# Optimization experiments

Hardware: AMD Instinct MI355X
Metric: run time of the kernel (lower is better)

The kernel has to match this reference:

```python
import jax, jax.numpy as jnp
import numpy as np

HEADS = 16

def setup_inputs() -> dict:
    key = jax.random.key(0)
    ks = jax.random.split(key, 5)
    B, T, D = 2, 2048, 2048
    s = 0.02
    return {
        "x": jax.random.normal(ks[0], (B, T, D), dtype=jnp.float32),
        "Wq": jax.random.normal(ks[1], (D, D), dtype=jnp.float32) * s,
        "Wk": jax.random.normal(ks[2], (D, D), dtype=jnp.float32) * s,
        "Wv": jax.random.normal(ks[3], (D, D), dtype=jnp.float32) * s,
        "Wo": jax.random.normal(ks[4], (D, D), dtype=jnp.float32) * s,
    }

def reference(x, Wq, Wk, Wv, Wo):
    B, T, _ = x.shape
    H = HEADS
    Dh = Wq.shape[1] // H
    # projections: [B,T,H,Dh]
    q = (x @ Wq).reshape(B, T, H, Dh)
    k = (x @ Wk).reshape(B, T, H, Dh)
    v = (x @ Wv).reshape(B, T, H, Dh)
    # raw scores [B,H,T,T]
    scores = jnp.einsum("bthd,bshd->bhts", q, k)
    # NOTE (faithful to source): mask is multiplicative 0/1 tril (the
    # masked_fill(-inf) in the torch code is not in-place and has no effect),
    # and the scale is sqrt(token_len), not sqrt(head_dim).
    mask = jnp.tril(jnp.ones((T, T), dtype=scores.dtype))
    scores = scores * mask
    attn = jax.nn.softmax(scores / (T ** 0.5), axis=-1)
    out = jnp.einsum("bhts,bshd->bthd", attn, v).reshape(B, T, H * Dh)
    return out @ Wo
```

## Files before the change

kernel.cpp:

```cpp
#include <hip/hip_runtime.h>


typedef __attribute__((ext_vector_type(4))) float  f32x4;
typedef __attribute__((ext_vector_type(8))) short  bf16x8;
typedef __attribute__((ext_vector_type(4))) unsigned short u16x4;

#define AS1 __attribute__((address_space(1)))
#define AS3 __attribute__((address_space(3)))

__device__ __forceinline__ void llds16(const void* g, void* l) {
  __builtin_amdgcn_global_load_lds((const AS1 void*)g, (AS3 void*)l, 16, 0, 0);
}

__device__ __forceinline__ unsigned short f2bf(float f) {
  unsigned int u = __builtin_bit_cast(unsigned int, f);
  u += 0x7fffu + ((u >> 16) & 1u);
  return (unsigned short)(u >> 16);
}

__device__ __forceinline__ unsigned short f2bfru(float f) {
  return (unsigned short)((__builtin_bit_cast(unsigned int, f) + 0x8000u) >> 16);
}

__device__ __forceinline__ float bf2f(unsigned short u) {
  return __builtin_bit_cast(float, (unsigned int)u << 16);
}

__global__ __launch_bounds__(256) void cast_x_kernel(const float* __restrict__ in,
                                                     unsigned short* __restrict__ out) {
  int i = blockIdx.x * 256 + threadIdx.x;
  f32x4 v = ((const f32x4*)in)[i];
  u16x4 o;
  o[0] = f2bf(v[0]); o[1] = f2bf(v[1]); o[2] = f2bf(v[2]); o[3] = f2bf(v[3]);
  ((u16x4*)out)[i] = o;
}

__global__ __launch_bounds__(256) void transpose_w4_kernel(
    const float* __restrict__ W0, const float* __restrict__ W1,
    const float* __restrict__ W2, const float* __restrict__ W3,
    unsigned short* __restrict__ T0, unsigned short* __restrict__ T1,
    unsigned short* __restrict__ T2, unsigned short* __restrict__ T3) {
  __shared__ float tile[32][33];
  const int z = blockIdx.z;
  const float* W = (z == 0) ? W0 : (z == 1) ? W1 : (z == 2) ? W2 : W3;
  unsigned short* Wt = (z == 0) ? T0 : (z == 1) ? T1 : (z == 2) ? T2 : T3;
  const int bx = blockIdx.x << 5;
  const int by = blockIdx.y << 5;
  const int tx = threadIdx.x;
  const int ty = threadIdx.y;
#pragma unroll
  for (int r = ty; r < 32; r += 8)
    tile[r][tx] = W[(size_t)(bx + r) * 2048 + by + tx];
  __syncthreads();
#pragma unroll
  for (int r = ty; r < 32; r += 8)
    Wt[(size_t)(by + r) * 2048 + bx + tx] = f2bf(tile[tx][r]);
}

__global__ __launch_bounds__(512, 2) void gemm_qkv8(const unsigned short* __restrict__ A,
                                                    const unsigned short* __restrict__ Bt,
                                                    unsigned short* __restrict__ Qb,
                                                    unsigned short* __restrict__ Kb,
                                                    unsigned short* __restrict__ Vt) {
  __shared__ __align__(16) char smem[131072];
  const int tid  = threadIdx.x;
  const int lane = tid & 63;
  const int w    = tid >> 6;
  const int wr   = w >> 2;
  const int wc   = w & 3;
  const int q16  = lane >> 4;
  const int l15  = lane & 15;
  const int f    = blockIdx.x;
  const int bn   = ((f & 7) << 1) + ((f >> 3) & 1);
  const int bm   = f >> 4;

  const int srow = tid >> 3;
  const int scl  = (tid & 7) ^ (srow & 7);
  const unsigned short* aS = A  + (size_t)((bm << 7) + srow) * 2048 + (scl << 3);
  const unsigned short* bS = Bt + (size_t)(bn * 384 + srow) * 2048 + (scl << 3);
  const int sdst = tid << 4;

  const int swzb = (q16 ^ (l15 & 7)) << 4;
  const int aRd  = ((wr << 6) + l15) << 7;
  const int bRd  = 16384 + ((wc * 96 + l15) << 7);

  f32x4 acc[4][6];
#pragma unroll
  for (int i = 0; i < 4; ++i)
#pragma unroll
    for (int j = 0; j < 6; ++j) acc[i][j] = (f32x4){0.f, 0.f, 0.f, 0.f};

  bf16x8 af[4], bf[3];

  auto TILE = [&](int kt, int cb, int ob, bool st) {
    const int kn = (kt + 1) << 6;
#pragma unroll
    for (int mi = 0; mi < 4; ++mi)
      af[mi] = *(const bf16x8*)(smem + cb + aRd + (mi << 11) + swzb);
#pragma unroll
    for (int r = 0; r < 3; ++r)
      bf[r] = *(const bf16x8*)(smem + cb + bRd + (r << 11) + swzb);
    if (st) {
      llds16(aS + kn,              smem + ob + sdst);
      llds16(aS + (1 << 17) + kn,  smem + ob + 8192 + sdst);
      llds16(bS + kn,              smem + ob + 16384 + sdst);
    }
    asm volatile("s_barrier" ::: "memory");
    __builtin_amdgcn_s_setprio(1);
#pragma unroll
    for (int mi = 0; mi < 4; ++mi)
#pragma unroll
      for (int r = 0; r < 3; ++r)
        acc[mi][r] = __builtin_amdgcn_mfma_f32_16x16x32_bf16(af[mi], bf[r], acc[mi][r], 0, 0, 0);
    __builtin_amdgcn_s_setprio(0);
    asm volatile("s_barrier" ::: "memory");
#pragma unroll
    for (int r = 0; r < 3; ++r)
      bf[r] = *(const bf16x8*)(smem + cb + bRd + ((3 + r) << 11) + swzb);
    if (st) {
      llds16(bS + (1 << 17) + kn,  smem + ob + 16384 + 8192 + sdst);
      llds16(bS + (2 << 17) + kn,  smem + ob + 16384 + 16384 + sdst);
      llds16(bS + (3 << 17) + kn,  smem + ob + 16384 + 24576 + sdst);
    }
    asm volatile("s_barrier" ::: "memory");
    __builtin_amdgcn_s_setprio(1);
#pragma unroll
    for (int mi = 0; mi < 4; ++mi)
#pragma unroll
      for (int r = 0; r < 3; ++r)
        acc[mi][3 + r] = __builtin_amdgcn_mfma_f32_16x16x32_bf16(af[mi], bf[r], acc[mi][3 + r], 0, 0, 0);
    __builtin_amdgcn_s_setprio(0);
    asm volatile("s_barrier" ::: "memory");
#pragma unroll
    for (int mi = 0; mi < 4; ++mi)
      af[mi] = *(const bf16x8*)(smem + cb + aRd + (mi << 11) + (swzb ^ 64));
#pragma unroll
    for (int r = 0; r < 3; ++r)
      bf[r] = *(const bf16x8*)(smem + cb + bRd + (r << 11) + (swzb ^ 64));
    if (st) {
      llds16(bS + (4 << 17) + kn,  smem + ob + 16384 + 32768 + sdst);
      llds16(bS + (5 << 17) + kn,  smem + ob + 16384 + 40960 + sdst);
    }
    asm volatile("s_barrier" ::: "memory");
    __builtin_amdgcn_s_setprio(1);
#pragma unroll
    for (int mi = 0; mi < 4; ++mi)
#pragma unroll
      for (int r = 0; r < 3; ++r)
        acc[mi][r] = __builtin_amdgcn_mfma_f32_16x16x32_bf16(af[mi], bf[r], acc[mi][r], 0, 0, 0);
    __builtin_amdgcn_s_setprio(0);
    asm volatile("s_barrier" ::: "memory");
#pragma unroll
    for (int r = 0; r < 3; ++r)
      bf[r] = *(const bf16x8*)(smem + cb + bRd + ((3 + r) << 11) + (swzb ^ 64));
    asm volatile("s_barrier" ::: "memory");
    __builtin_amdgcn_s_setprio(1);
#pragma unroll
    for (int mi = 0; mi < 4; ++mi)
#pragma unroll
      for (int r = 0; r < 3; ++r)
        acc[mi][3 + r] = __builtin_amdgcn_mfma_f32_16x16x32_bf16(af[mi], bf[r], acc[mi][3 + r], 0, 0, 0);
    __builtin_amdgcn_s_setprio(0);
    asm volatile("s_barrier" ::: "memory");
    asm volatile("s_waitcnt vmcnt(0)" ::: "memory");
    asm volatile("s_barrier" ::: "memory");
  };

  llds16(aS, smem + sdst);
  llds16(aS + (1 << 17), smem + 8192 + sdst);
#pragma unroll
  for (int li = 0; li < 6; ++li)
    llds16(bS + li * (1 << 17), smem + 16384 + li * 8192 + sdst);
  asm volatile("s_waitcnt vmcnt(0)" ::: "memory");
  asm volatile("s_barrier" ::: "memory");

#pragma unroll 1
  for (int kt = 0; kt < 30; kt += 2) {
    TILE(kt,     0,     65536, true);
    TILE(kt + 1, 65536, 0,     true);
  }
  TILE(30, 0,     65536, true);
  TILE(31, 65536, 0,     false);

  const float qscale = 0.02209708691207961f;
  const int rb = q16 << 2;
#pragma unroll
  for (int mi = 0; mi < 4; ++mi) {
    int m0 = (bm << 7) + (wr << 6) + (mi << 4) + rb;
#pragma unroll
    for (int ni = 0; ni < 6; ++ni) {
      int gn = bn * 384 + wc * 96 + (ni << 4) + l15;
      int region = gn >> 11;
      int nloc = gn & 2047;
      if (region == 0) {
#pragma unroll
        for (int j = 0; j < 4; ++j)
          Qb[(size_t)(m0 + j) * 2048 + nloc] = f2bf(acc[mi][ni][j] * qscale);
      } else if (region == 1) {
#pragma unroll
        for (int j = 0; j < 4; ++j)
          Kb[(size_t)(m0 + j) * 2048 + nloc] = f2bf(acc[mi][ni][j]);
      } else {
        u16x4 pk;
#pragma unroll
        for (int j = 0; j < 4; ++j) pk[j] = f2bf(acc[mi][ni][j]);
        int b = m0 >> 11, t = m0 & 2047;
        *(u16x4*)(Vt + ((size_t)((b << 4) + (nloc >> 7)) * 128 + (nloc & 127)) * 2048 + t) = pk;
      }
    }
  }
}

__global__ __launch_bounds__(256, 2) void gemm_wo(const unsigned short* __restrict__ A,
                                                  const unsigned short* __restrict__ Bt,
                                                  float* __restrict__ Co) {
  constexpr int SLOT = 8192 + 8192;
  __shared__ __align__(16) char smem[3 * SLOT];

  const int tid  = threadIdx.x;
  const int lane = tid & 63;
  const int w    = tid >> 6;
  const int q16  = lane >> 4;
  const int l15  = lane & 15;
  const int f    = blockIdx.x;
  const int g    = f >> 3;
  const int bn   = ((f & 7) << 1) + (g & 1);
  const int bm   = g >> 1;
  const int wmb  = (w >> 1) << 6;
  const int wnb  = (w & 1) << 6;

  f32x4 acc[4][4];
#pragma unroll
  for (int i = 0; i < 4; ++i)
#pragma unroll
    for (int j = 0; j < 4; ++j) acc[i][j] = (f32x4){0.f, 0.f, 0.f, 0.f};

  const int rowA = tid >> 2;
  const int chA  = tid & 3;
  auto stageT = [&](int t, char* sb) {
    const int k0 = t << 5;
#pragma unroll
    for (int r = 0; r < 2; ++r) {
      int row = (r << 6) + rowA;
      const unsigned short* src = A + (size_t)((bm << 7) + row) * 2048 + k0
                                    + ((chA ^ ((row >> 1) & 3)) << 3);
      llds16(src, sb + (r << 12) + (w << 10));
    }
#pragma unroll
    for (int r = 0; r < 2; ++r) {
      int row = (r << 6) + rowA;
      const unsigned short* src = Bt + (size_t)((bn << 7) + row) * 2048 + k0
                                     + ((chA ^ ((row >> 1) & 3)) << 3);
      llds16(src, sb + 8192 + (r << 12) + (w << 10));
    }
  };

  auto computeT = [&](const char* base) {
    bf16x8 af[4], bf[4];
#pragma unroll
    for (int mi = 0; mi < 4; ++mi) {
      int row = wmb + (mi << 4) + l15;
      af[mi] = *(const bf16x8*)(base + (row << 6) + ((q16 ^ ((row >> 1) & 3)) << 4));
    }
#pragma unroll
    for (int ni = 0; ni < 4; ++ni) {
      int row = wnb + (ni << 4) + l15;
      bf[ni] = *(const bf16x8*)(base + 8192 + (row << 6) + ((q16 ^ ((row >> 1) & 3)) << 4));
    }
    __builtin_amdgcn_s_setprio(1);
#pragma unroll
    for (int mi = 0; mi < 4; ++mi)
#pragma unroll
      for (int ni = 0; ni < 4; ++ni)
        acc[mi][ni] = __builtin_amdgcn_mfma_f32_16x16x32_bf16(af[mi], bf[ni], acc[mi][ni], 0, 0, 0);
    __builtin_amdgcn_s_setprio(0);
  };

  auto STEP = [&](int t, char* cbase, char* sbase) {
    asm volatile("s_waitcnt vmcnt(4)" ::: "memory");
    __builtin_amdgcn_s_barrier();
    stageT(t + 2, sbase);
    computeT(cbase);
  };

  char* s0 = smem;
  char* s1 = smem + SLOT;
  char* s2 = smem + 2 * SLOT;

  stageT(0, s0); stageT(1, s1);
#pragma unroll 1
  for (int t = 0; t < 60; t += 3) {
    STEP(t,     s0, s2);
    STEP(t + 1, s1, s0);
    STEP(t + 2, s2, s1);
  }
  STEP(60, s0, s2);
  STEP(61, s1, s0);
  asm volatile("s_waitcnt vmcnt(4)" ::: "memory");
  __builtin_amdgcn_s_barrier();
  computeT(s2);
  asm volatile("s_waitcnt vmcnt(0)" ::: "memory");
  __builtin_amdgcn_s_barrier();
  computeT(s0);

  const int rb = q16 << 2;
#pragma unroll
  for (int mi = 0; mi < 4; ++mi) {
    int m0 = (bm << 7) + wmb + (mi << 4) + rb;
#pragma unroll
    for (int ni = 0; ni < 4; ++ni) {
      int n = (bn << 7) + wnb + (ni << 4) + l15;
#pragma unroll
      for (int j = 0; j < 4; ++j)
        Co[(size_t)(m0 + j) * 2048 + n] = acc[mi][ni][j];
    }
  }
}

__global__ __launch_bounds__(256) void vsuf_kernel(const unsigned short* __restrict__ Vt,
                                                   float* __restrict__ Suf) {
  const int row  = blockIdx.x * 4 + (threadIdx.x >> 6);
  const int lane = threadIdx.x & 63;
  const unsigned short* vp = Vt + (size_t)row * 2048 + (lane << 5);
  float a = 0.f;
#pragma unroll
  for (int c = 0; c < 4; ++c) {
    bf16x8 v = *(const bf16x8*)(vp + (c << 3));
#pragma unroll
    for (int j = 0; j < 8; ++j) a += bf2f((unsigned short)v[j]);
  }
  float I = a;
#pragma unroll
  for (int off = 1; off < 64; off <<= 1) {
    float t = __shfl_down(I, off, 64);
    I += (lane + off < 64) ? t : 0.f;
  }
  Suf[(size_t)lane * 4096 + row] = I;
  if (lane == 0) Suf[(size_t)64 * 4096 + row] = 0.f;
}

__global__ __launch_bounds__(256) void attn_kernel(const unsigned short* __restrict__ Q,
                                                   const unsigned short* __restrict__ K,
                                                   const unsigned short* __restrict__ V,
                                                   const float* __restrict__ Suf,
                                                   unsigned short* __restrict__ O) {
  __shared__ __align__(16) char smem[36864];
  const int tid  = threadIdx.x;
  const int lane = tid & 63;
  const int w    = tid >> 6;
  const int q16  = lane >> 4;
  const int l15  = lane & 15;
  const int f    = blockIdx.x;
  const int bh    = ((f & 7) << 2) + ((f >> 3) & 3);
  const int strip = 31 - (f >> 5);
  const int b  = bh >> 4;
  const size_t qkbase = ((size_t)(b << 11)) * 2048 + ((size_t)(bh & 15) << 7);
  const size_t vbase  = (size_t)bh << 18;
  const int rb = q16 << 2;
  char* Psm = smem + 32768 + (w << 10);

  const int numIter = 2 * strip + 2;
  const int t0 = (strip << 6) + (w << 4);

  auto stage = [&](int s0, int kb, int vb) {
#pragma unroll
    for (int c = 0; c < 2; ++c) {
      int ch = (w << 1) + c;
      int rowK = (ch << 2) + q16;
      int colbK = (l15 << 4) ^ ((rowK & 7) << 4);
      llds16(K + qkbase + (size_t)(s0 + rowK) * 2048 + (colbK >> 1), smem + kb + (ch << 10));
      int rowV = (ch << 4) + (lane >> 2);
      int colbV = ((lane & 3) << 4) ^ (((rowV >> 2) & 3) << 4);
      llds16(V + vbase + (size_t)rowV * 2048 + s0 + (colbV >> 1), smem + vb + (ch << 10));
    }
  };

  bf16x8 qf[4];
  {
    const unsigned short* qp = Q + qkbase + (size_t)(t0 + l15) * 2048 + (q16 << 3);
#pragma unroll
    for (int kk = 0; kk < 4; ++kk) qf[kk] = *(const bf16x8*)(qp + (kk << 5));
  }

  f32x4 oacc[8];
#pragma unroll
  for (int i = 0; i < 8; ++i) oacc[i] = (f32x4){0.f, 0.f, 0.f, 0.f};
  float ell[4] = {0.f, 0.f, 0.f, 0.f};

  stage(0, 0, 16384);
  asm volatile("s_waitcnt vmcnt(0)" ::: "memory");
  __syncthreads();

  int cur = 0;
  for (int it = 0; it < numIter; ++it) {
    const int s0 = it << 5;
    if (it + 1 < numIter)
      stage(s0 + 32, (cur ^ 1) << 13, 16384 + ((cur ^ 1) << 13));

    if (s0 <= t0) {
      const int kb = cur << 13;
      const int vb = 16384 + (cur << 13);

      f32x4 sA = (f32x4){0.f, 0.f, 0.f, 0.f}, sB = (f32x4){0.f, 0.f, 0.f, 0.f};
#pragma unroll
      for (int kk = 0; kk < 4; ++kk) {
        int r0 = l15;
        bf16x8 k0f = *(const bf16x8*)(smem + kb + (r0 << 8) + (((kk << 6) + (q16 << 4)) ^ ((r0 & 7) << 4)));
        sA = __builtin_amdgcn_mfma_f32_16x16x32_bf16(qf[kk], k0f, sA, 0, 0, 0);
        int r1 = 16 + l15;
        bf16x8 k1f = *(const bf16x8*)(smem + kb + (r1 << 8) + (((kk << 6) + (q16 << 4)) ^ ((r1 & 7) << 4)));
        sB = __builtin_amdgcn_mfma_f32_16x16x32_bf16(qf[kk], k1f, sB, 0, 0, 0);
      }

      float pA[4], pB[4];
      if (s0 + 31 <= t0) {
#pragma unroll
        for (int j = 0; j < 4; ++j) {
          pA[j] = __expf(sA[j]);
          pB[j] = __expf(sB[j]);
          ell[j] += pA[j] + pB[j];
        }
      } else {
#pragma unroll
        for (int j = 0; j < 4; ++j) {
          int t  = t0 + rb + j;
          int sa = s0 + l15;
          float vA = (sa <= t)      ? sA[j] : 0.f;
          float vB = (sa + 16 <= t) ? sB[j] : 0.f;
          pA[j] = __expf(vA);
          pB[j] = __expf(vB);
          ell[j] += pA[j] + pB[j];
        }
      }

#pragma unroll
      for (int j = 0; j < 4; ++j) {
        int r   = rb + j;
        int swz = ((r >> 1) & 3) << 4;
        *(unsigned short*)(Psm + (r << 6) + ((l15 << 1) ^ swz))        = f2bfru(pA[j]);
        *(unsigned short*)(Psm + (r << 6) + ((32 + (l15 << 1)) ^ swz)) = f2bfru(pB[j]);
      }
      asm volatile("s_waitcnt lgkmcnt(0)" ::: "memory");

      bf16x8 pa;
      {
        int r = l15;
        pa = *(const bf16x8*)(Psm + (r << 6) + ((q16 << 4) ^ (((r >> 1) & 3) << 4)));
      }
#pragma unroll
      for (int ni = 0; ni < 8; ++ni) {
        int dr = (ni << 4) + l15;
        bf16x8 vbf = *(const bf16x8*)(smem + vb + (dr << 6) + ((q16 << 4) ^ (((dr >> 2) & 3) << 4)));
        oacc[ni] = __builtin_amdgcn_mfma_f32_16x16x32_bf16(pa, vbf, oacc[ni], 0, 0, 0);
      }
    }

    asm volatile("s_waitcnt vmcnt(0)" ::: "memory");
    __syncthreads();
    cur ^= 1;
  }

  const int send = (t0 & ~31) + 32;
  const float* sp = Suf + (size_t)(send >> 5) * 4096 + ((size_t)bh << 7);
  const float extra = (float)(2048 - send);
#pragma unroll
  for (int ni = 0; ni < 8; ++ni) {
    float sv = sp[(ni << 4) + l15];
#pragma unroll
    for (int j = 0; j < 4; ++j) oacc[ni][j] += sv;
  }

#pragma unroll
  for (int j = 0; j < 4; ++j) {
    float r = ell[j];
    r += __shfl_xor(r, 1, 64);
    r += __shfl_xor(r, 2, 64);
    r += __shfl_xor(r, 4, 64);
    r += __shfl_xor(r, 8, 64);
    float inv = 1.0f / (r + extra);
    int t = t0 + rb + j;
    unsigned short* op = O + qkbase + (size_t)t * 2048;
#pragma unroll
    for (int ni = 0; ni < 8; ++ni)
      op[(ni << 4) + l15] = f2bf(oacc[ni][j] * inv);
  }
}

extern "C" void kernel_launch(void* const* d_in, const int* in_sizes, int n_in,
                              void* d_out, int out_size, void* d_ws, size_t ws_size,
                              hipStream_t stream) {
  (void)in_sizes; (void)n_in; (void)out_size; (void)ws_size;
  const float* x  = (const float*)d_in[0];
  const float* Wq = (const float*)d_in[1];
  const float* Wk = (const float*)d_in[2];
  const float* Wv = (const float*)d_in[3];
  const float* Wo = (const float*)d_in[4];
  float* out = (float*)d_out;

  char* ws = (char*)d_ws;
  unsigned short* Xb  = (unsigned short*)(ws);
  unsigned short* Wqt = (unsigned short*)(ws + 16777216);
  unsigned short* Wkt = (unsigned short*)(ws + 16777216 + 8388608);
  unsigned short* Wvt = (unsigned short*)(ws + 16777216 + 2 * 8388608);
  unsigned short* Wot = (unsigned short*)(ws + 16777216 + 3 * 8388608);
  unsigned short* Qb  = (unsigned short*)(ws + 50331648);
  unsigned short* Kb  = (unsigned short*)(ws + 67108864);
  unsigned short* Vt  = (unsigned short*)(ws + 83886080);
  unsigned short* Ob  = Xb;
  float*          Suf = (float*)Wqt;

  cast_x_kernel<<<8192, 256, 0, stream>>>(x, Xb);
  {
    dim3 tb(32, 8), tg(64, 64, 4);
    transpose_w4_kernel<<<tg, tb, 0, stream>>>(Wq, Wk, Wv, Wo, Wqt, Wkt, Wvt, Wot);
  }
  gemm_qkv8<<<512, 512, 0, stream>>>(Xb, Wqt, Qb, Kb, Vt);

  vsuf_kernel<<<1024, 256, 0, stream>>>(Vt, Suf);

  attn_kernel<<<1024, 256, 0, stream>>>(Qb, Kb, Vt, Suf, Ob);

  gemm_wo<<<512, 256, 0, stream>>>(Ob, Wot, out);
}
```

Before: 257.0 us.

## Restructure QKV GEMM to 128x256 tiles with triple-buffered LDS pipeline

Replaces the 128x384-tile QKV projection GEMM, which double-buffered its LDS and hand-interleaved loads with many barriers, by a 128x256 tile using three LDS slots. Loads for tile k+2 are issued while tile k computes, with one vmcnt wait and one barrier per K step. The grid grows from 512 to 768 blocks with a new block-to-tile mapping. Each block gets less data reuse and a smaller accumulator, in exchange for fewer synchronisation points, deeper prefetch and more blocks.

```diff
diff --git a/kernel.cpp b/kernel.cpp
--- a/kernel.cpp
+++ b/kernel.cpp
@@ -57,12 +57,13 @@
     Wt[(size_t)(by + r) * 2048 + bx + tx] = f2bf(tile[tx][r]);
 }
 
-__global__ __launch_bounds__(512, 2) void gemm_qkv8(const unsigned short* __restrict__ A,
-                                                    const unsigned short* __restrict__ Bt,
-                                                    unsigned short* __restrict__ Qb,
-                                                    unsigned short* __restrict__ Kb,
-                                                    unsigned short* __restrict__ Vt) {
-  __shared__ __align__(16) char smem[131072];
+__global__ __launch_bounds__(512, 2) void gemm_qkv(const unsigned short* __restrict__ A,
+                                                   const unsigned short* __restrict__ Bt,
+                                                   unsigned short* __restrict__ Qb,
+                                                   unsigned short* __restrict__ Kb,
+                                                   unsigned short* __restrict__ Vt) {
+  constexpr int SLOT = 49152;
+  __shared__ __align__(16) char smem[3 * SLOT];
   const int tid  = threadIdx.x;
   const int lane = tid & 63;
   const int w    = tid >> 6;
@@ -71,116 +72,82 @@
   const int q16  = lane >> 4;
   const int l15  = lane & 15;
   const int f    = blockIdx.x;
-  const int bn   = ((f & 7) << 1) + ((f >> 3) & 1);
-  const int bm   = f >> 4;
+  const int g    = f >> 3;
+  const int bn   = (f & 7) * 3 + (g % 3);
+  const int bm   = g / 3;
 
   const int srow = tid >> 3;
   const int scl  = (tid & 7) ^ (srow & 7);
   const unsigned short* aS = A  + (size_t)((bm << 7) + srow) * 2048 + (scl << 3);
-  const unsigned short* bS = Bt + (size_t)(bn * 384 + srow) * 2048 + (scl << 3);
+  const unsigned short* bS = Bt + (size_t)(bn * 256 + srow) * 2048 + (scl << 3);
   const int sdst = tid << 4;
 
   const int swzb = (q16 ^ (l15 & 7)) << 4;
   const int aRd  = ((wr << 6) + l15) << 7;
-  const int bRd  = 16384 + ((wc * 96 + l15) << 7);
-
-  f32x4 acc[4][6];
+  const int bRd  = 16384 + ((wc << 6) + l15) << 7 == 0 ? 0 : 16384 + (((wc << 6) + l15) << 7);
+
+  f32x4 acc[4][4];
 #pragma unroll
   for (int i = 0; i < 4; ++i)
 #pragma unroll
-    for (int j = 0; j < 6; ++j) acc[i][j] = (f32x4){0.f, 0.f, 0.f, 0.f};
-
-  bf16x8 af[4], bf[3];
-
-  auto TILE = [&](int kt, int cb, int ob, bool st) {
-    const int kn = (kt + 1) << 6;
-#pragma unroll
-    for (int mi = 0; mi < 4; ++mi)
-      af[mi] = *(const bf16x8*)(smem + cb + aRd + (mi << 11) + swzb);
-#pragma unroll
-    for (int r = 0; r < 3; ++r)
-      bf[r] = *(const bf16x8*)(smem + cb + bRd + (r << 11) + swzb);
-    if (st) {
-      llds16(aS + kn,              smem + ob + sdst);
-      llds16(aS + (1 << 17) + kn,  smem + ob + 8192 + sdst);
-      llds16(bS + kn,              smem + ob + 16384 + sdst);
-    }
-    asm volatile("s_barrier" ::: "memory");
-    __builtin_amdgcn_s_setprio(1);
-#pragma unroll
-    for (int mi = 0; mi < 4; ++mi)
-#pragma unroll
-      for (int r = 0; r < 3; ++r)
-        acc[mi][r] = __builtin_amdgcn_mfma_f32_16x16x32_bf16(af[mi], bf[r], acc[mi][r], 0, 0, 0);
-    __builtin_amdgcn_s_setprio(0);
-    asm volatile("s_barrier" ::: "memory");
-#pragma unroll
-    for (int r = 0; r < 3; ++r)
-      bf[r] = *(const bf16x8*)(smem + cb + bRd + ((3 + r) << 11) + swzb);
-    if (st) {
-      llds16(bS + (1 << 17) + kn,  smem + ob + 16384 + 8192 + sdst);
-      llds16(bS + (2 << 17) + kn,  smem + ob + 16384 + 16384 + sdst);
-      llds16(bS + (3 << 17) + kn,  smem + ob + 16384 + 24576 + sdst);
-    }
-    asm volatile("s_barrier" ::: "memory");
-    __builtin_amdgcn_s_setprio(1);
-#pragma unroll
-    for (int mi = 0; mi < 4; ++mi)
-#pragma unroll
-      for (int r = 0; r < 3; ++r)
-        acc[mi][3 + r] = __builtin_amdgcn_mfma_f32_16x16x32_bf16(af[mi], bf[r], acc[mi][3 + r], 0, 0, 0);
-    __builtin_amdgcn_s_setprio(0);
-    asm volatile("s_barrier" ::: "memory");
-#pragma unroll
-    for (int mi = 0; mi < 4; ++mi)
-      af[mi] = *(const bf16x8*)(smem + cb + aRd + (mi << 11) + (swzb ^ 64));
-#pragma unroll
-    for (int r = 0; r < 3; ++r)
-      bf[r] = *(const bf16x8*)(smem + cb + bRd + (r << 11) + (swzb ^ 64));
-    if (st) {
-      llds16(bS + (4 << 17) + kn,  smem + ob + 16384 + 32768 + sdst);
-      llds16(bS + (5 << 17) + kn,  smem + ob + 16384 + 40960 + sdst);
-    }
-    asm volatile("s_barrier" ::: "memory");
-    __builtin_amdgcn_s_setprio(1);
-#pragma unroll
-    for (int mi = 0; mi < 4; ++mi)
-#pragma unroll
-      for (int r = 0; r < 3; ++r)
-        acc[mi][r] = __builtin_amdgcn_mfma_f32_16x16x32_bf16(af[mi], bf[r], acc[mi][r], 0, 0, 0);
-    __builtin_amdgcn_s_setprio(0);
-    asm volatile("s_barrier" ::: "memory");
-#pragma unroll
-    for (int r = 0; r < 3; ++r)
-      bf[r] = *(const bf16x8*)(smem + cb + bRd + ((3 + r) << 11) + (swzb ^ 64));
-    asm volatile("s_barrier" ::: "memory");
-    __builtin_amdgcn_s_setprio(1);
-#pragma unroll
-    for (int mi = 0; mi < 4; ++mi)
-#pragma unroll
-      for (int r = 0; r < 3; ++r)
-        acc[mi][3 + r] = __builtin_amdgcn_mfma_f32_16x16x32_bf16(af[mi], bf[r], acc[mi][3 + r], 0, 0, 0);
-    __builtin_amdgcn_s_setprio(0);
-    asm volatile("s_barrier" ::: "memory");
-    asm volatile("s_waitcnt vmcnt(0)" ::: "memory");
-    asm volatile("s_barrier" ::: "memory");
-  };
-
-  llds16(aS, smem + sdst);
-  llds16(aS + (1 << 17), smem + 8192 + sdst);
-#pragma unroll
-  for (int li = 0; li < 6; ++li)
-    llds16(bS + li * (1 << 17), smem + 16384 + li * 8192 + sdst);
-  asm volatile("s_waitcnt vmcnt(0)" ::: "memory");
-  asm volatile("s_barrier" ::: "memory");
-
+    for (int j = 0; j < 4; ++j) acc[i][j] = (f32x4){0.f, 0.f, 0.f, 0.f};
+
+  auto stageT = [&](int kt, char* sb) {
+    const size_t ko = (size_t)kt << 6;
+    llds16(aS + ko,              sb + sdst);
+    llds16(aS + (64 * 2048) + ko, sb + 8192 + sdst);
+#pragma unroll
+    for (int r = 0; r < 4; ++r)
+      llds16(bS + (size_t)r * (64 * 2048) + ko, sb + 16384 + (r << 13) + sdst);
+  };
+
+  auto computeT = [&](const char* base) {
+#pragma unroll
+    for (int ks = 0; ks < 2; ++ks) {
+      const int sw = swzb ^ (ks << 6);
+      bf16x8 af[4], bf[4];
+#pragma unroll
+      for (int mi = 0; mi < 4; ++mi)
+        af[mi] = *(const bf16x8*)(base + aRd + (mi << 11) + sw);
+#pragma unroll
+      for (int ni = 0; ni < 4; ++ni)
+        bf[ni] = *(const bf16x8*)(base + 16384 + (((wc << 6) + l15) << 7) + (ni << 11) + sw);
+      __builtin_amdgcn_s_setprio(1);
+#pragma unroll
+      for (int mi = 0; mi < 4; ++mi)
+#pragma unroll
+        for (int ni = 0; ni < 4; ++ni)
+          acc[mi][ni] = __builtin_amdgcn_mfma_f32_16x16x32_bf16(af[mi], bf[ni], acc[mi][ni], 0, 0, 0);
+      __builtin_amdgcn_s_setprio(0);
+    }
+  };
+
+  char* s0 = smem;
+  char* s1 = smem + SLOT;
+  char* s2 = smem + 2 * SLOT;
+
+#define W6()  asm volatile("s_waitcnt vmcnt(6)" ::: "memory")
+#define W0()  asm volatile("s_waitcnt vmcnt(0)" ::: "memory")
+#define BAR() __builtin_amdgcn_s_barrier()
+
+  stageT(0, s0); stageT(1, s1);
+  W6(); BAR();
+  stageT(2, s2);
+  computeT(s0);
 #pragma unroll 1
-  for (int kt = 0; kt < 30; kt += 2) {
-    TILE(kt,     0,     65536, true);
-    TILE(kt + 1, 65536, 0,     true);
-  }
-  TILE(30, 0,     65536, true);
-  TILE(31, 65536, 0,     false);
+  for (int b = 1; b <= 25; b += 3) {
+    W6(); BAR(); stageT(b + 2, s0); computeT(s1);
+    W6(); BAR(); stageT(b + 3, s1); computeT(s2);
+    W6(); BAR(); stageT(b + 4, s2); computeT(s0);
+  }
+  W6(); BAR(); stageT(30, s0); computeT(s1);
+  W6(); BAR(); stageT(31, s1); computeT(s2);
+  W6(); BAR(); computeT(s0);
+  W0(); BAR(); computeT(s1);
+
+#undef W6
+#undef W0
+#undef BAR
 
   const float qscale = 0.02209708691207961f;
   const int rb = q16 << 2;
@@ -188,8 +155,8 @@
   for (int mi = 0; mi < 4; ++mi) {
     int m0 = (bm << 7) + (wr << 6) + (mi << 4) + rb;
 #pragma unroll
-    for (int ni = 0; ni < 6; ++ni) {
-      int gn = bn * 384 + wc * 96 + (ni << 4) + l15;
+    for (int ni = 0; ni < 4; ++ni) {
+      int gn = (bn << 8) + (wc << 6) + (ni << 4) + l15;
       int region = gn >> 11;
       int nloc = gn & 2047;
       if (region == 0) {
@@ -514,7 +481,7 @@
     dim3 tb(32, 8), tg(64, 64, 4);
     transpose_w4_kernel<<<tg, tb, 0, stream>>>(Wq, Wk, Wv, Wo, Wqt, Wkt, Wvt, Wot);
   }
-  gemm_qkv8<<<512, 512, 0, stream>>>(Xb, Wqt, Qb, Kb, Vt);
+  gemm_qkv<<<768, 512, 0, stream>>>(Xb, Wqt, Qb, Kb, Vt);
 
   vsuf_kernel<<<1024, 256, 0, stream>>>(Vt, Suf);
 
```

Result: slower. 265.7 us (+3.4%).
